# Kernel optimization log

Hardware: AMD Instinct MI355X
Metric: run time of the kernel (lower is better)

Reference implementation:

```python
import jax, jax.numpy as jnp
import numpy as np

B = 8; NPC = 12500; N = B * NPC
L = 10.0; RES = 0.7; K = 16
IN_CH = 64; H1 = 68; H2 = 128; RNN = 128; ATTN = 32; E4 = 4 * RNN
EPS = 1e-5


def _knn_np(refs, queries, k):
    out = np.empty((queries.shape[0], k), dtype=np.int64)
    r2 = (refs * refs).sum(1)
    for s in range(0, queries.shape[0], 2048):
        q = queries[s:s + 2048]
        d2 = (q * q).sum(1)[:, None] - 2.0 * q @ refs.T + r2[None, :]
        out[s:s + q.shape[0]] = np.argpartition(d2, k, axis=1)[:, :k]
    return out


def setup_inputs():
    rng = np.random.default_rng(0)
    pos = rng.uniform(0.0, L, (N, 3)).astype(np.float32)
    batch = np.repeat(np.arange(B), NPC).astype(np.int32)
    x = (0.5 * rng.standard_normal((N, IN_CH))).astype(np.float32)
    refl = rng.uniform(0.0, 1.0, N).astype(np.float32)
    # voxel-grid sampling: one representative point per occupied voxel per cloud
    G = int(np.ceil(L / RES)) + 1
    v = np.floor(pos / RES).astype(np.int64)
    vkey = ((batch.astype(np.int64) * G + v[:, 0]) * G + v[:, 1]) * G + v[:, 2]
    _, first = np.unique(vkey, return_index=True)
    idx = np.sort(first)
    M = idx.shape[0]
    # per-cloud brute-force KNN (k neighbors in full set for every sampled point)
    src_list = []
    for b in range(B):
        qi = idx[(idx >= b * NPC) & (idx < (b + 1) * NPC)]
        src_list.append(_knn_np(pos[b * NPC:(b + 1) * NPC], pos[qi], K) + b * NPC)
    src = np.concatenate(src_list, 0).reshape(-1)
    tgt = np.repeat(np.arange(M), K)
    edge_index = np.stack([src, tgt]).astype(np.int32)

    def W(*s):
        return jnp.asarray((0.05 * rng.standard_normal(s)).astype(np.float32))

    def zeros(c):
        return jnp.zeros((c,), jnp.float32)

    def bnp(c):  # packed inference-mode BN params: [gamma, beta, mean, var]
        return jnp.asarray(np.stack([1.0 + 0.1 * rng.standard_normal(c), 0.1 * rng.standard_normal(c), 0.1 * rng.standard_normal(c), 1.0 + 0.1 * rng.uniform(0.0, 1.0, c)]).astype(np.float32))

    def dwp(c):  # depthwise k=1 conv = per-channel [weight, bias]
        return jnp.asarray(np.stack([1.0 + 0.1 * rng.standard_normal(c), 0.1 * rng.standard_normal(c)]).astype(np.float32))

    gum = -np.log(-np.log(rng.uniform(1e-6, 1.0 - 1e-6, (B, 2))))
    return dict(
        x=jnp.asarray(x), pos=jnp.asarray(pos), reflectance=jnp.asarray(refl),
        gumbel=jnp.asarray(gum.astype(np.float32)),
        gate_w1=W(4, H1), gate_b1=zeros(H1), gate_w2=W(H1, H1), gate_b2=zeros(H1),
        gate_wg=W(H1, 2), gate_bg=jnp.asarray(np.array([0.0, 2.0], np.float32)),
        loc_w1=W(H1, H2), loc_b1=zeros(H2), loc_w2=W(H2, H2), loc_b2=zeros(H2),
        attn_w1=W(H2, ATTN), attn_b1=zeros(ATTN), attn_w2=W(ATTN),
        exp_w=W(RNN, E4), exp_b=zeros(E4), exp_bn=bnp(E4),
        ds1_dw=dwp(E4), ds1_bn1=bnp(E4), ds1_pw_w=W(E4, E4), ds1_pw_b=zeros(E4), ds1_bn2=bnp(E4),
        blk_bn1=bnp(E4),
        ds2_dw=dwp(E4), ds2_bn1=bnp(E4), ds2_pw_w=W(E4, E4), ds2_pw_b=zeros(E4), ds2_bn2=bnp(E4),
        blk_bn2=bnp(E4),
        proj_w=W(E4, RNN), proj_b=zeros(RNN), proj_bn=bnp(RNN),
        batch=jnp.asarray(batch), idx=jnp.asarray(idx.astype(np.int32)),
        edge_index=jnp.asarray(edge_index), k=K, num_graphs=B)


def _bn(z, p):
    return p[0] * (z - p[2]) / jnp.sqrt(p[3] + EPS) + p[1]


def reference(x, pos, reflectance, gumbel, gate_w1, gate_b1, gate_w2, gate_b2, gate_wg, gate_bg, loc_w1, loc_b1, loc_w2, loc_b2, attn_w1, attn_b1, attn_w2, exp_w, exp_b, exp_bn, ds1_dw, ds1_bn1, ds1_pw_w, ds1_pw_b, ds1_bn2, blk_bn1, ds2_dw, ds2_bn1, ds2_pw_w, ds2_pw_b, ds2_bn2, blk_bn2, proj_w, proj_b, proj_bn, batch, idx, edge_index, k, num_graphs):
    # --- BinaryReflectanceGate (soft gumbel-softmax, tau=1) ---
    feats = jnp.concatenate([pos, reflectance[:, None]], -1)  # [N,4]
    h = jax.nn.relu(feats @ gate_w1 + gate_b1)
    h = jax.nn.relu(h @ gate_w2 + gate_b2)
    pooled = jax.ops.segment_max(h, batch, num_segments=num_graphs)  # global_max_pool
    logits = pooled @ gate_wg + gate_bg
    y_soft = jax.nn.softmax(logits + gumbel, axis=-1)
    refl_g = y_soft[:, 1][batch] * reflectance  # gated reflectance [N]
    pos4 = jnp.concatenate([pos, refl_g[:, None]], -1)  # [N,4]
    # --- AttentivePointNetConv: gather -> local MLP -> softmax attn -> reduce ---
    M = idx.shape[0]
    src = edge_index[0].reshape(M, k)  # k source neighbors per centroid
    msg_in = jnp.concatenate([x[src], pos4[src] - pos4[idx][:, None, :]], -1)  # [M,k,68]
    hm = jax.nn.relu(msg_in @ loc_w1 + loc_b1)
    msg = jax.nn.relu(hm @ loc_w2 + loc_b2)  # [M,k,128]
    score = jnp.tanh(msg @ attn_w1 + attn_b1) @ attn_w2  # [M,k]
    alpha = jax.nn.softmax(score, axis=-1)  # softmax over each centroid's edges
    agg = jnp.einsum('mk,mkc->mc', alpha, msg)  # [M,128]
    # --- InvertedResidualBlock (all convs kernel=1 -> channel matmuls, BN inference) ---
    out = jax.nn.relu(_bn(agg @ exp_w + exp_b, exp_bn))  # expand 128->512

    def ds(z, dw, bn1, pw_w, pw_b, bn2):
        d = jax.nn.relu(_bn(z * dw[0] + dw[1], bn1))  # depthwise k=1
        return _bn(d @ pw_w + pw_b, bn2)  # pointwise

    out = _bn(ds(out, ds1_dw, ds1_bn1, ds1_pw_w, ds1_pw_b, ds1_bn2), blk_bn1)
    out = _bn(ds(out, ds2_dw, ds2_bn1, ds2_pw_w, ds2_pw_b, ds2_bn2), blk_bn2)
    out = _bn(out @ proj_w + proj_b, proj_bn)  # project 512->128
    out = jax.nn.relu(out + agg)  # identity shortcut (RNN==RNN)
    return (out, pos[idx], batch[idx], refl_g[idx])
```

## Files before the change

kernel.cpp:

```cpp
#include <hip/hip_runtime.h>
#include <hip/hip_bf16.h>

typedef __hip_bfloat16 bf16;

#define B_GR 8
#define IN_CH 64
#define H1 68
#define H2 128
#define ATTN 32
#define E4 512
#define RNN 128
#define KNN 16
#define EPSV 1e-5f

typedef __attribute__((ext_vector_type(8))) short s8v;
typedef __attribute__((ext_vector_type(4))) float f4v;
#define MFMA16(a,b,c) __builtin_amdgcn_mfma_f32_16x16x32_bf16(a,b,c,0,0,0)

#define SK96 104
#define SK128 136
#define SK512 520

template<int DT> __device__ __forceinline__ float LD(const void* p, size_t i) {
    if (DT) return __bfloat162float(((const bf16*)p)[i]);
    return ((const float*)p)[i];
}
template<int DT> __device__ __forceinline__ void ST(void* p, size_t i, float v) {
    if (DT) ((bf16*)p)[i] = __float2bfloat16(v);
    else    ((float*)p)[i] = v;
}
__device__ __forceinline__ unsigned short f2bfb(float f) {
    unsigned u = __float_as_uint(f);
    unsigned r = (u + 0x7FFFu + ((u >> 16) & 1u)) >> 16;
    return (unsigned short)r;
}
__device__ __forceinline__ float bfb2f(unsigned short u) {
    return __uint_as_float(((unsigned)u) << 16);
}

__global__ void prep_kernel(const void* pos, int* flag, int* pooled) {
    const int tid = threadIdx.x;
    for (int i = tid; i < B_GR*H1; i += 256) pooled[i] = 0;
    if (tid == 0) {
        const unsigned* w = (const unsigned*)pos;
        int ok = 1;
        #pragma unroll 8
        for (int i = 0; i < 256; i++) {
            float f = __uint_as_float((w[i] & 0xFFFFu) << 16);
            if (!(f >= -0.01f && f <= 10.05f)) ok = 0;
        }
        *flag = ok;
    }
}

#define W1T_E (128*SK96)
#define W2T_E (128*SK128)
#define AW1T_E (32*SK128)
#define EXPT_E (512*SK128)
#define D1T_E (512*SK512)
#define D2T_E (512*SK512)
#define PJT_E (128*SK512)
#define GW2T_E (80*SK96)
template<int DT> __global__ __launch_bounds__(256) void trans_kernel(
    const int* __restrict__ flag,
    const void* __restrict__ w1, const void* __restrict__ w2, const void* __restrict__ aw1,
    const void* __restrict__ expw, const void* __restrict__ d1pw,
    const void* __restrict__ d2pw, const void* __restrict__ pjw,
    const void* __restrict__ gw2,
    unsigned short* __restrict__ w1T, unsigned short* __restrict__ w2T,
    unsigned short* __restrict__ aw1T, unsigned short* __restrict__ expwT,
    unsigned short* __restrict__ d1pwT, unsigned short* __restrict__ d2pwT,
    unsigned short* __restrict__ pjwT, unsigned short* __restrict__ gw2gT)
{
    if (*flag != DT) return;
    const int T0 = W1T_E, T1 = T0+W2T_E, T2 = T1+AW1T_E, T3 = T2+EXPT_E,
              T4 = T3+D1T_E, T5 = T4+D2T_E, T6 = T5+PJT_E, T7 = T6+GW2T_E;
    for (int i = blockIdx.x*256 + threadIdx.x; i < T7; i += gridDim.x*256) {
        if (i < T0) {
            int n = i / SK96, k = i - n*SK96;
            w1T[i] = (k < H1) ? f2bfb(LD<DT>(w1, (size_t)k*H2 + n)) : 0;
        } else if (i < T1) {
            int j = i - T0; int n = j / SK128, k = j - n*SK128;
            w2T[j] = (k < H2) ? f2bfb(LD<DT>(w2, (size_t)k*H2 + n)) : 0;
        } else if (i < T2) {
            int j = i - T1; int n = j / SK128, k = j - n*SK128;
            aw1T[j] = (k < H2) ? f2bfb(LD<DT>(aw1, (size_t)k*ATTN + n)) : 0;
        } else if (i < T3) {
            int j = i - T2; int n = j / SK128, k = j - n*SK128;
            expwT[j] = (k < RNN) ? f2bfb(LD<DT>(expw, (size_t)k*E4 + n)) : 0;
        } else if (i < T4) {
            int j = i - T3; int n = j / SK512, k = j - n*SK512;
            d1pwT[j] = (k < E4) ? f2bfb(LD<DT>(d1pw, (size_t)k*E4 + n)) : 0;
        } else if (i < T5) {
            int j = i - T4; int n = j / SK512, k = j - n*SK512;
            d2pwT[j] = (k < E4) ? f2bfb(LD<DT>(d2pw, (size_t)k*E4 + n)) : 0;
        } else if (i < T6) {
            int j = i - T5; int n = j / SK512, k = j - n*SK512;
            pjwT[j] = (k < E4) ? f2bfb(LD<DT>(pjw, (size_t)k*RNN + n)) : 0;
        } else {
            int j = i - T6; int n = j / SK96, k = j - n*SK96;
            gw2gT[j] = (k < H1 && n < H1) ? f2bfb(LD<DT>(gw2, (size_t)k*H1 + n)) : 0;
        }
    }
}

template<int DT> __global__ void coef_kernel(
    const int* __restrict__ flag,
    const void* __restrict__ expb, const void* __restrict__ expbn,
    const void* __restrict__ d1dw, const void* __restrict__ d1bn1,
    const void* __restrict__ d1pb, const void* __restrict__ d1bn2, const void* __restrict__ bbn1,
    const void* __restrict__ d2dw, const void* __restrict__ d2bn1,
    const void* __restrict__ d2pb, const void* __restrict__ d2bn2, const void* __restrict__ bbn2,
    const void* __restrict__ pjb, const void* __restrict__ pjbn,
    float4* __restrict__ C1, float2* __restrict__ C2, float2* __restrict__ C3,
    float2* __restrict__ C4)
{
    if (*flag != DT) return;
    int c = blockIdx.x*256 + threadIdx.x;
    if (c < E4) {
        float a_e = LD<DT>(expbn,c) * rsqrtf(LD<DT>(expbn,3*E4+c)+EPSV);
        float t0  = a_e*(LD<DT>(expb,c) - LD<DT>(expbn,2*E4+c)) + LD<DT>(expbn,E4+c);
        float a1 = LD<DT>(d1bn1,c) * rsqrtf(LD<DT>(d1bn1,3*E4+c)+EPSV);
        float s1 = a1 * LD<DT>(d1dw,c);
        float t1 = a1*(LD<DT>(d1dw,E4+c) - LD<DT>(d1bn1,2*E4+c)) + LD<DT>(d1bn1,E4+c);
        C1[c] = make_float4(a_e, t0, s1, t1);
        float a2 = LD<DT>(d1bn2,c) * rsqrtf(LD<DT>(d1bn2,3*E4+c)+EPSV);
        float t2 = a2*(LD<DT>(d1pb,c) - LD<DT>(d1bn2,2*E4+c)) + LD<DT>(d1bn2,E4+c);
        float a3 = LD<DT>(bbn1,c) * rsqrtf(LD<DT>(bbn1,3*E4+c)+EPSV);
        float S2 = a3*a2;
        float T2 = a3*(t2 - LD<DT>(bbn1,2*E4+c)) + LD<DT>(bbn1,E4+c);
        float a4 = LD<DT>(d2bn1,c) * rsqrtf(LD<DT>(d2bn1,3*E4+c)+EPSV);
        float sdw = a4 * LD<DT>(d2dw,c);
        float tdw = a4*(LD<DT>(d2dw,E4+c) - LD<DT>(d2bn1,2*E4+c)) + LD<DT>(d2bn1,E4+c);
        C2[c] = make_float2(sdw*S2, sdw*T2 + tdw);
        float a5 = LD<DT>(d2bn2,c) * rsqrtf(LD<DT>(d2bn2,3*E4+c)+EPSV);
        float t5 = a5*(LD<DT>(d2pb,c) - LD<DT>(d2bn2,2*E4+c)) + LD<DT>(d2bn2,E4+c);
        float a6 = LD<DT>(bbn2,c) * rsqrtf(LD<DT>(bbn2,3*E4+c)+EPSV);
        C3[c] = make_float2(a6*a5, a6*(t5 - LD<DT>(bbn2,2*E4+c)) + LD<DT>(bbn2,E4+c));
    }
    if (c < RNN) {
        float ap = LD<DT>(pjbn,c) * rsqrtf(LD<DT>(pjbn,3*RNN+c)+EPSV);
        C4[c] = make_float2(ap, ap*(LD<DT>(pjb,c) - LD<DT>(pjbn,2*RNN+c)) + LD<DT>(pjbn,RNN+c));
    }
}

template<int DT> __global__ __launch_bounds__(256) void gate_mfma(
    const int* __restrict__ flag,
    const void* __restrict__ pos, const void* __restrict__ refl,
    const void* __restrict__ w1, const void* __restrict__ b1, const void* __restrict__ b2g,
    const unsigned short* __restrict__ gw2gT,
    int* __restrict__ pooled, int NPC, int CPB)
{
    if (*flag != DT) return;
    __shared__ __align__(16) unsigned short hs[256*SK96];
    __shared__ float w1s[4*H1], b1s[H1], b2s[H1];
    const int tid = threadIdx.x;
    for (int i = tid; i < 4*H1; i += 256) w1s[i] = LD<DT>(w1, i);
    if (tid < H1) { b1s[tid] = LD<DT>(b1, tid); b2s[tid] = LD<DT>(b2g, tid); }
    __syncthreads();

    const int bb = blockIdx.x / CPB;
    const int cc = blockIdx.x % CPB;
    const int base = bb*NPC + cc*256;
    const int limit = NPC - cc*256;
    const int p = base + ((tid < limit) ? tid : 0);

    {
        float f0 = LD<DT>(pos, (size_t)p*3+0), f1 = LD<DT>(pos, (size_t)p*3+1);
        float f2 = LD<DT>(pos, (size_t)p*3+2), f3 = LD<DT>(refl, p);
        float h[H1];
        #pragma unroll
        for (int j = 0; j < H1; j++)
            h[j] = fmaxf(b1s[j] + f0*w1s[j] + f1*w1s[H1+j] + f2*w1s[2*H1+j] + f3*w1s[3*H1+j], 0.f);
        #pragma unroll
        for (int j = 0; j < H1; j += 2) {
            unsigned v = (unsigned)f2bfb(h[j]) | ((unsigned)f2bfb(h[j+1]) << 16);
            *(unsigned*)&hs[tid*SK96 + j] = v;
        }
        #pragma unroll
        for (int j = H1; j < 96; j += 2) *(unsigned*)&hs[tid*SK96 + j] = 0;
    }
    __syncthreads();

    const int wv = tid >> 6, lane = tid & 63, quad = lane >> 4, l15 = lane & 15;
    f4v acc[4][5];
    #pragma unroll
    for (int mt = 0; mt < 4; mt++)
        #pragma unroll
        for (int nt = 0; nt < 5; nt++) acc[mt][nt] = (f4v){0.f,0.f,0.f,0.f};
    s8v af[4][3];
    #pragma unroll
    for (int mt = 0; mt < 4; mt++)
        #pragma unroll
        for (int ks = 0; ks < 3; ks++)
            af[mt][ks] = *(const s8v*)&hs[(wv*64 + mt*16 + l15)*SK96 + ks*32 + quad*8];
    #pragma unroll
    for (int nt = 0; nt < 5; nt++) {
        #pragma unroll
        for (int ks = 0; ks < 3; ks++) {
            s8v bf_ = *(const s8v*)&gw2gT[(size_t)(nt*16 + l15)*SK96 + ks*32 + quad*8];
            #pragma unroll
            for (int mt = 0; mt < 4; mt++) acc[mt][nt] = MFMA16(af[mt][ks], bf_, acc[mt][nt]);
        }
    }
    #pragma unroll
    for (int nt = 0; nt < 5; nt++) {
        int col = nt*16 + l15;
        float v = acc[0][nt][0];
        #pragma unroll
        for (int mt = 0; mt < 4; mt++)
            #pragma unroll
            for (int r = 0; r < 4; r++) v = fmaxf(v, acc[mt][nt][r]);
        v = fmaxf(v, __shfl_xor(v, 16));
        v = fmaxf(v, __shfl_xor(v, 32));
        if (quad == 0 && col < H1) {
            float o = fmaxf(v + b2s[col], 0.f);
            atomicMax(&pooled[bb*H1 + col], __float_as_int(o));
        }
    }
}

template<int DT> __global__ void gate2_kernel(
    const int* __restrict__ flag, const int* __restrict__ pooled,
    const void* __restrict__ wg, const void* __restrict__ bg,
    const void* __restrict__ gum, float* __restrict__ y1)
{
    if (*flag != DT) return;
    __shared__ float lg[B_GR][2];
    const int t = threadIdx.x;
    if (t < B_GR*2) {
        int b = t >> 1, g = t & 1;
        float a = LD<DT>(bg, g) + LD<DT>(gum, b*2+g);
        for (int c = 0; c < H1; c++) a += __int_as_float(pooled[b*H1+c]) * LD<DT>(wg, c*2+g);
        lg[b][g] = a;
    }
    __syncthreads();
    if (t < B_GR) {
        float l0 = lg[t][0], l1 = lg[t][1];
        float m = fmaxf(l0, l1);
        float e0 = __expf(l0-m), e1 = __expf(l1-m);
        y1[t] = e1 / (e0 + e1);
    }
}

template<int DT> __global__ __launch_bounds__(256) void edge_mfma(
    const int* __restrict__ flag,
    const void* __restrict__ x, const void* __restrict__ pos,
    const void* __restrict__ refl, const float* __restrict__ y1,
    const int* __restrict__ batch,
    const int* __restrict__ idxarr, const int* __restrict__ esrc,
    const void* __restrict__ b1, const void* __restrict__ b2,
    const void* __restrict__ ab1, const void* __restrict__ aw2,
    const unsigned short* __restrict__ gw1T, const unsigned short* __restrict__ gw2T,
    const unsigned short* __restrict__ gaw1T,
    void* __restrict__ out, int M)
{
    if (*flag != DT) return;
    __shared__ __align__(16) unsigned short u2[128*SK128];
    __shared__ __align__(16) unsigned short Hs[128*SK128];
    __shared__ float p4[8][4];
    __shared__ int   srow[128];
    __shared__ float b1s[H2], b2s[H2], ab1s[ATTN], aw2s[ATTN];
    __shared__ float scores[128], alpha[128];
    float* att = (float*)Hs;

    const int tid = threadIdx.x;
    const int m0 = blockIdx.x * 8;

    if (tid < 128) {
        int mm = m0 + (tid >> 4); if (mm >= M) mm = M - 1;
        srow[tid] = esrc[mm*KNN + (tid & 15)];
    }
    if (tid < 32) {
        int tt = tid >> 2, c = tid & 3;
        int mm = m0 + tt; if (mm >= M) mm = M - 1;
        int t_idx = idxarr[mm];
        p4[tt][c] = (c < 3) ? LD<DT>(pos, (size_t)t_idx*3 + c)
                            : y1[batch[t_idx]] * LD<DT>(refl, t_idx);
    }
    if (tid < H2) { b1s[tid] = LD<DT>(b1, tid); b2s[tid] = LD<DT>(b2, tid); }
    if (tid < ATTN) { ab1s[tid] = LD<DT>(ab1, tid); aw2s[tid] = LD<DT>(aw2, tid); }
    __syncthreads();

    if (DT) {
        int r = tid >> 1, hf = tid & 1;
        int s = srow[r], tt = r >> 4;
        const uint4* xs = (const uint4*)x;
        uint4* du = (uint4*)u2;
        #pragma unroll
        for (int q = 0; q < 4; q++)
            du[r*13 + hf*4 + q] = xs[(size_t)s*8 + hf*4 + q];
        if (hf == 0) {
            #pragma unroll
            for (int k = 64; k < 68; k++) {
                float v = (k < 67) ? LD<1>(pos, (size_t)s*3 + (k-64)) - p4[tt][k-64]
                                   : y1[batch[s]] * LD<1>(refl, s) - p4[tt][3];
                u2[r*SK96 + k] = f2bfb(v);
            }
        } else {
            #pragma unroll
            for (int k = 68; k < 96; k += 2) *(unsigned*)&u2[r*SK96 + k] = 0;
        }
    } else {
        int r = tid >> 1, half = tid & 1;
        int s = srow[r], tt = r >> 4;
        size_t xb = (size_t)s * IN_CH;
        int k0 = half * 48;
        for (int kk = 0; kk < 48; kk++) {
            int k = k0 + kk;
            float v;
            if (k < IN_CH)       v = LD<DT>(x, xb + k);
            else if (k < 67)     v = LD<DT>(pos, (size_t)s*3 + (k - 64)) - p4[tt][k - 64];
            else if (k == 67)    v = y1[batch[s]] * LD<DT>(refl, s) - p4[tt][3];
            else                 v = 0.f;
            u2[r*SK96 + k] = f2bfb(v);
        }
    }
    __syncthreads();

    const int wv = tid >> 6, lane = tid & 63, quad = lane >> 4, l15 = lane & 15;
    const int rbase = wv * 32;

    {
        f4v acc[2][8];
        #pragma unroll
        for (int mt = 0; mt < 2; mt++)
            #pragma unroll
            for (int nt = 0; nt < 8; nt++) acc[mt][nt] = (f4v){0.f,0.f,0.f,0.f};
        s8v af[2][3];
        #pragma unroll
        for (int mt = 0; mt < 2; mt++)
            #pragma unroll
            for (int ks = 0; ks < 3; ks++)
                af[mt][ks] = *(const s8v*)&u2[(rbase + mt*16 + l15)*SK96 + ks*32 + quad*8];
        #pragma unroll
        for (int nt = 0; nt < 8; nt++) {
            #pragma unroll
            for (int ks = 0; ks < 3; ks++) {
                s8v bf_ = *(const s8v*)&gw1T[(size_t)(nt*16 + l15)*SK96 + ks*32 + quad*8];
                acc[0][nt] = MFMA16(af[0][ks], bf_, acc[0][nt]);
                acc[1][nt] = MFMA16(af[1][ks], bf_, acc[1][nt]);
            }
        }
        #pragma unroll
        for (int mt = 0; mt < 2; mt++)
            #pragma unroll
            for (int nt = 0; nt < 8; nt++)
                #pragma unroll
                for (int r = 0; r < 4; r++) {
                    int row = rbase + mt*16 + quad*4 + r;
                    int col = nt*16 + l15;
                    Hs[row*SK128 + col] = f2bfb(fmaxf(acc[mt][nt][r] + b1s[col], 0.f));
                }
    }
    __syncthreads();

    {
        f4v acc[2][8];
        #pragma unroll
        for (int mt = 0; mt < 2; mt++)
            #pragma unroll
            for (int nt = 0; nt < 8; nt++) acc[mt][nt] = (f4v){0.f,0.f,0.f,0.f};
        s8v af[2][4];
        #pragma unroll
        for (int mt = 0; mt < 2; mt++)
            #pragma unroll
            for (int ks = 0; ks < 4; ks++)
                af[mt][ks] = *(const s8v*)&Hs[(rbase + mt*16 + l15)*SK128 + ks*32 + quad*8];
        #pragma unroll
        for (int nt = 0; nt < 8; nt++) {
            #pragma unroll
            for (int ks = 0; ks < 4; ks++) {
                s8v bf_ = *(const s8v*)&gw2T[(size_t)(nt*16 + l15)*SK128 + ks*32 + quad*8];
                acc[0][nt] = MFMA16(af[0][ks], bf_, acc[0][nt]);
                acc[1][nt] = MFMA16(af[1][ks], bf_, acc[1][nt]);
            }
        }
        #pragma unroll
        for (int mt = 0; mt < 2; mt++)
            #pragma unroll
            for (int nt = 0; nt < 8; nt++)
                #pragma unroll
                for (int r = 0; r < 4; r++) {
                    int row = rbase + mt*16 + quad*4 + r;
                    int col = nt*16 + l15;
                    u2[row*SK128 + col] = f2bfb(fmaxf(acc[mt][nt][r] + b2s[col], 0.f));
                }
    }
    __syncthreads();

    {
        f4v acc[2][2];
        #pragma unroll
        for (int mt = 0; mt < 2; mt++)
            #pragma unroll
            for (int nt = 0; nt < 2; nt++) acc[mt][nt] = (f4v){0.f,0.f,0.f,0.f};
        s8v af[2][4];
        #pragma unroll
        for (int mt = 0; mt < 2; mt++)
            #pragma unroll
            for (int ks = 0; ks < 4; ks++)
                af[mt][ks] = *(const s8v*)&u2[(rbase + mt*16 + l15)*SK128 + ks*32 + quad*8];
        #pragma unroll
        for (int nt = 0; nt < 2; nt++) {
            #pragma unroll
            for (int ks = 0; ks < 4; ks++) {
                s8v bf_ = *(const s8v*)&gaw1T[(size_t)(nt*16 + l15)*SK128 + ks*32 + quad*8];
                acc[0][nt] = MFMA16(af[0][ks], bf_, acc[0][nt]);
                acc[1][nt] = MFMA16(af[1][ks], bf_, acc[1][nt]);
            }
        }
        #pragma unroll
        for (int mt = 0; mt < 2; mt++)
            #pragma unroll
            for (int nt = 0; nt < 2; nt++)
                #pragma unroll
                for (int r = 0; r < 4; r++) {
                    int row = rbase + mt*16 + quad*4 + r;
                    int col = nt*16 + l15;
                    att[row*ATTN + col] = tanhf(acc[mt][nt][r] + ab1s[col]) * aw2s[col];
                }
    }
    __syncthreads();

    if (tid < 128) {
        float s = 0.f;
        const f4v* row = (const f4v*)&att[tid*ATTN];
        #pragma unroll
        for (int i = 0; i < 8; i++) { f4v v = row[i]; s += v[0]+v[1]+v[2]+v[3]; }
        scores[tid] = s;
    }
    __syncthreads();
    if (tid < 128) {
        int base = (tid >> 4) << 4;
        float mx = scores[base];
        #pragma unroll
        for (int j = 1; j < KNN; j++) mx = fmaxf(mx, scores[base+j]);
        float den = 0.f;
        #pragma unroll
        for (int j = 0; j < KNN; j++) den += __expf(scores[base+j] - mx);
        alpha[tid] = __expf(scores[tid] - mx) / den;
    }
    __syncthreads();

    for (int o = tid; o < 1024; o += 256) {
        int tt = o >> 7, c = o & 127;
        int mm = m0 + tt;
        if (mm < M) {
            float a = 0.f;
            #pragma unroll
            for (int j = 0; j < KNN; j++)
                a += alpha[tt*16 + j] * bfb2f(u2[(tt*16 + j)*SK128 + c]);
            ST<DT>(out, (size_t)mm*H2 + c, a);
        }
    }
    if (tid < 32) {
        int tt = tid >> 2, c = tid & 3;
        int mm = m0 + tt;
        if (mm < M) {
            if (c < 3) ST<DT>(out, (size_t)M*128 + mm*3 + c, p4[tt][c]);
            else {
                ST<DT>(out, (size_t)M*131 + mm, (float)batch[idxarr[mm]]);
                ST<DT>(out, (size_t)M*132 + mm, p4[tt][3]);
            }
        }
    }
}

template<int DT> __global__ __launch_bounds__(256) void post_mfma(
    const int* __restrict__ flag,
    const unsigned short* __restrict__ expwT, const unsigned short* __restrict__ d1pwT,
    const unsigned short* __restrict__ d2pwT, const unsigned short* __restrict__ pjwT,
    const float4* __restrict__ C1, const float2* __restrict__ C2,
    const float2* __restrict__ C3, const float2* __restrict__ C4,
    void* __restrict__ out, int M)
{
    if (*flag != DT) return;
    __shared__ __align__(16) unsigned short zs[32*SK512];
    __shared__ __align__(16) unsigned short a0[32*SK128];
    const int tid = threadIdx.x;
    const int m0 = blockIdx.x * 32;

    {
        int r = tid >> 3;
        int c0 = (tid & 7) * 16;
        int mm = m0 + r;
        for (int c = c0; c < c0+16; c++) {
            float v = (mm < M) ? LD<DT>(out, (size_t)mm*RNN + c) : 0.f;
            a0[r*SK128 + c] = f2bfb(v);
        }
        if ((tid & 7) == 7) for (int c = RNN; c < SK128; c++) a0[r*SK128 + c] = 0;
    }
    __syncthreads();

    const int wv = tid >> 6, lane = tid & 63, quad = lane >> 4, l15 = lane & 15;
    const int nbase = wv * 128;

    f4v acc[2][8];

    #pragma unroll
    for (int mt = 0; mt < 2; mt++)
        #pragma unroll
        for (int nt = 0; nt < 8; nt++) acc[mt][nt] = (f4v){0.f,0.f,0.f,0.f};
    #pragma unroll
    for (int ks = 0; ks < 4; ks++) {
        s8v af0 = *(const s8v*)&a0[(l15)*SK128 + ks*32 + quad*8];
        s8v af1 = *(const s8v*)&a0[(16+l15)*SK128 + ks*32 + quad*8];
        #pragma unroll
        for (int nt = 0; nt < 8; nt++) {
            s8v bf_ = *(const s8v*)&expwT[(size_t)(nbase + nt*16 + l15)*SK128 + ks*32 + quad*8];
            acc[0][nt] = MFMA16(af0, bf_, acc[0][nt]);
            acc[1][nt] = MFMA16(af1, bf_, acc[1][nt]);
        }
    }
    #pragma unroll
    for (int nt = 0; nt < 8; nt++) {
        int col = nbase + nt*16 + l15;
        float4 cf = C1[col];
        #pragma unroll
        for (int mt = 0; mt < 2; mt++)
            #pragma unroll
            for (int r = 0; r < 4; r++) {
                int row = mt*16 + quad*4 + r;
                float u = fmaxf(cf.x*acc[mt][nt][r] + cf.y, 0.f);
                float d = fmaxf(cf.z*u + cf.w, 0.f);
                zs[row*SK512 + col] = f2bfb(d);
            }
    }
    __syncthreads();

    #pragma unroll
    for (int mt = 0; mt < 2; mt++)
        #pragma unroll
        for (int nt = 0; nt < 8; nt++) acc[mt][nt] = (f4v){0.f,0.f,0.f,0.f};
    for (int ks = 0; ks < 16; ks++) {
        s8v af0 = *(const s8v*)&zs[(l15)*SK512 + ks*32 + quad*8];
        s8v af1 = *(const s8v*)&zs[(16+l15)*SK512 + ks*32 + quad*8];
        #pragma unroll
        for (int nt = 0; nt < 8; nt++) {
            s8v bf_ = *(const s8v*)&d1pwT[(size_t)(nbase + nt*16 + l15)*SK512 + ks*32 + quad*8];
            acc[0][nt] = MFMA16(af0, bf_, acc[0][nt]);
            acc[1][nt] = MFMA16(af1, bf_, acc[1][nt]);
        }
    }
    __syncthreads();
    #pragma unroll
    for (int nt = 0; nt < 8; nt++) {
        int col = nbase + nt*16 + l15;
        float2 cf = C2[col];
        #pragma unroll
        for (int mt = 0; mt < 2; mt++)
            #pragma unroll
            for (int r = 0; r < 4; r++) {
                int row = mt*16 + quad*4 + r;
                zs[row*SK512 + col] = f2bfb(fmaxf(cf.x*acc[mt][nt][r] + cf.y, 0.f));
            }
    }
    __syncthreads();

    #pragma unroll
    for (int mt = 0; mt < 2; mt++)
        #pragma unroll
        for (int nt = 0; nt < 8; nt++) acc[mt][nt] = (f4v){0.f,0.f,0.f,0.f};
    for (int ks = 0; ks < 16; ks++) {
        s8v af0 = *(const s8v*)&zs[(l15)*SK512 + ks*32 + quad*8];
        s8v af1 = *(const s8v*)&zs[(16+l15)*SK512 + ks*32 + quad*8];
        #pragma unroll
        for (int nt = 0; nt < 8; nt++) {
            s8v bf_ = *(const s8v*)&d2pwT[(size_t)(nbase + nt*16 + l15)*SK512 + ks*32 + quad*8];
            acc[0][nt] = MFMA16(af0, bf_, acc[0][nt]);
            acc[1][nt] = MFMA16(af1, bf_, acc[1][nt]);
        }
    }
    __syncthreads();
    #pragma unroll
    for (int nt = 0; nt < 8; nt++) {
        int col = nbase + nt*16 + l15;
        float2 cf = C3[col];
        #pragma unroll
        for (int mt = 0; mt < 2; mt++)
            #pragma unroll
            for (int r = 0; r < 4; r++) {
                int row = mt*16 + quad*4 + r;
                zs[row*SK512 + col] = f2bfb(cf.x*acc[mt][nt][r] + cf.y);
            }
    }
    __syncthreads();

    {
        f4v pacc[2][2];
        #pragma unroll
        for (int mt = 0; mt < 2; mt++)
            #pragma unroll
            for (int nt = 0; nt < 2; nt++) pacc[mt][nt] = (f4v){0.f,0.f,0.f,0.f};
        for (int ks = 0; ks < 16; ks++) {
            s8v af0 = *(const s8v*)&zs[(l15)*SK512 + ks*32 + quad*8];
            s8v af1 = *(const s8v*)&zs[(16+l15)*SK512 + ks*32 + quad*8];
            #pragma unroll
            for (int nt = 0; nt < 2; nt++) {
                s8v bf_ = *(const s8v*)&pjwT[(size_t)(wv*32 + nt*16 + l15)*SK512 + ks*32 + quad*8];
                pacc[0][nt] = MFMA16(af0, bf_, pacc[0][nt]);
                pacc[1][nt] = MFMA16(af1, bf_, pacc[1][nt]);
            }
        }
        #pragma unroll
        for (int nt = 0; nt < 2; nt++) {
            int col = wv*32 + nt*16 + l15;
            float2 cf = C4[col];
            #pragma unroll
            for (int mt = 0; mt < 2; mt++)
                #pragma unroll
                for (int r = 0; r < 4; r++) {
                    int row = mt*16 + quad*4 + r;
                    int mm = m0 + row;
                    if (mm < M) {
                        float agv = bfb2f(a0[row*SK128 + col]);
                        float o = fmaxf(cf.x*pacc[mt][nt][r] + cf.y + agv, 0.f);
                        ST<DT>(out, (size_t)mm*RNN + col, o);
                    }
                }
        }
    }
}

extern "C" void kernel_launch(void* const* d_in, const int* in_sizes, int n_in,
                              void* d_out, int out_size, void* d_ws, size_t ws_size,
                              hipStream_t stream)
{
    const void* x    = d_in[0];
    const void* pos  = d_in[1];
    const void* refl = d_in[2];
    const void* gum  = d_in[3];
    const void* gw1  = d_in[4];
    const void* gb1  = d_in[5];
    const void* gw2  = d_in[6];
    const void* gb2  = d_in[7];
    const void* gwg  = d_in[8];
    const void* gbg  = d_in[9];
    const void* lw1  = d_in[10];
    const void* lb1  = d_in[11];
    const void* lw2  = d_in[12];
    const void* lb2  = d_in[13];
    const void* aw1  = d_in[14];
    const void* ab1  = d_in[15];
    const void* aw2  = d_in[16];
    const void* expw = d_in[17];
    const void* expb = d_in[18];
    const void* expbn= d_in[19];
    const void* d1dw = d_in[20];
    const void* d1bn1= d_in[21];
    const void* d1pw = d_in[22];
    const void* d1pb = d_in[23];
    const void* d1bn2= d_in[24];
    const void* bbn1 = d_in[25];
    const void* d2dw = d_in[26];
    const void* d2bn1= d_in[27];
    const void* d2pw = d_in[28];
    const void* d2pb = d_in[29];
    const void* d2bn2= d_in[30];
    const void* bbn2 = d_in[31];
    const void* pjw  = d_in[32];
    const void* pjb  = d_in[33];
    const void* pjbn = d_in[34];
    const int* batch = (const int*)d_in[35];
    const int* idxp  = (const int*)d_in[36];
    const int* eidx  = (const int*)d_in[37];

    const int N = in_sizes[2];
    const int M = in_sizes[36];
    const int NPC = N / B_GR;
    const int CPB = (NPC + 255) / 256;

    char* wsb = (char*)d_ws;
    int*  flag   = (int*)wsb;
    int*  pooled = (int*)(wsb + 16);
    float* y1    = (float*)(wsb + 2304);
    unsigned short* w1T   = (unsigned short*)(wsb + 2368);
    unsigned short* w2T   = w1T + W1T_E;
    unsigned short* aw1T  = w2T + W2T_E;
    unsigned short* expwT = aw1T + AW1T_E;
    unsigned short* d1pwT = expwT + EXPT_E;
    unsigned short* d2pwT = d1pwT + D1T_E;
    unsigned short* pjwT  = d2pwT + D2T_E;
    unsigned short* gw2gT = pjwT + PJT_E;
    float4* C1 = (float4*)(gw2gT + GW2T_E + 8);
    float2* C2 = (float2*)(C1 + E4);
    float2* C3 = C2 + E4;
    float2* C4 = C3 + E4;

    prep_kernel<<<1, 256, 0, stream>>>(pos, flag, pooled);

    trans_kernel<0><<<512, 256, 0, stream>>>(flag, lw1, lw2, aw1, expw, d1pw, d2pw, pjw, gw2,
                                             w1T, w2T, aw1T, expwT, d1pwT, d2pwT, pjwT, gw2gT);
    trans_kernel<1><<<512, 256, 0, stream>>>(flag, lw1, lw2, aw1, expw, d1pw, d2pw, pjw, gw2,
                                             w1T, w2T, aw1T, expwT, d1pwT, d2pwT, pjwT, gw2gT);

    coef_kernel<0><<<2, 256, 0, stream>>>(flag, expb, expbn, d1dw, d1bn1, d1pb, d1bn2, bbn1,
                                          d2dw, d2bn1, d2pb, d2bn2, bbn2, pjb, pjbn,
                                          C1, C2, C3, C4);
    coef_kernel<1><<<2, 256, 0, stream>>>(flag, expb, expbn, d1dw, d1bn1, d1pb, d1bn2, bbn1,
                                          d2dw, d2bn1, d2pb, d2bn2, bbn2, pjb, pjbn,
                                          C1, C2, C3, C4);

    gate_mfma<0><<<B_GR*CPB, 256, 0, stream>>>(flag, pos, refl, gw1, gb1, gb2, gw2gT, pooled, NPC, CPB);
    gate_mfma<1><<<B_GR*CPB, 256, 0, stream>>>(flag, pos, refl, gw1, gb1, gb2, gw2gT, pooled, NPC, CPB);

    gate2_kernel<0><<<1, 64, 0, stream>>>(flag, pooled, gwg, gbg, gum, y1);
    gate2_kernel<1><<<1, 64, 0, stream>>>(flag, pooled, gwg, gbg, gum, y1);

    const int EB = (M + 7) / 8;
    edge_mfma<0><<<EB, 256, 0, stream>>>(flag, x, pos, refl, y1, batch, idxp, eidx,
                                         lb1, lb2, ab1, aw2, w1T, w2T, aw1T, d_out, M);
    edge_mfma<1><<<EB, 256, 0, stream>>>(flag, x, pos, refl, y1, batch, idxp, eidx,
                                         lb1, lb2, ab1, aw2, w1T, w2T, aw1T, d_out, M);

    const int PB = (M + 31) / 32;
    post_mfma<0><<<PB, 256, 0, stream>>>(flag, expwT, d1pwT, d2pwT, pjwT, C1, C2, C3, C4, d_out, M);
    post_mfma<1><<<PB, 256, 0, stream>>>(flag, expwT, d1pwT, d2pwT, pjwT, C1, C2, C3, C4, d_out, M);
}
```

Baseline: 532.0 us.

## Reuse one LDS buffer across MLP stages, fuse score reduction via shuffles, vectorize aggregation

Drops the second 128x136 bf16 shared buffer so every MLP stage reads from and writes back into the same buffer. Each stage loads its A fragments into registers and syncs before overwriting, which halves LDS use per block and should allow more resident blocks per CU. The attention score sum is now done with lane shuffles in registers instead of a shared scratch array, removing one LDS round trip and a barrier. The final alpha-weighted aggregation reads 8 bf16 values per load and writes with 16-byte stores; the cost is extra barriers between stages.

```diff
diff --git a/kernel.cpp b/kernel.cpp
--- a/kernel.cpp
+++ b/kernel.cpp
@@ -257,12 +257,10 @@
 {
     if (*flag != DT) return;
     __shared__ __align__(16) unsigned short u2[128*SK128];
-    __shared__ __align__(16) unsigned short Hs[128*SK128];
     __shared__ float p4[8][4];
     __shared__ int   srow[128];
     __shared__ float b1s[H2], b2s[H2], ab1s[ATTN], aw2s[ATTN];
     __shared__ float scores[128], alpha[128];
-    float* att = (float*)Hs;
 
     const int tid = threadIdx.x;
     const int m0 = blockIdx.x * 8;
@@ -289,17 +287,17 @@
         uint4* du = (uint4*)u2;
         #pragma unroll
         for (int q = 0; q < 4; q++)
-            du[r*13 + hf*4 + q] = xs[(size_t)s*8 + hf*4 + q];
+            du[r*17 + hf*4 + q] = xs[(size_t)s*8 + hf*4 + q];
         if (hf == 0) {
             #pragma unroll
             for (int k = 64; k < 68; k++) {
                 float v = (k < 67) ? LD<1>(pos, (size_t)s*3 + (k-64)) - p4[tt][k-64]
                                    : y1[batch[s]] * LD<1>(refl, s) - p4[tt][3];
-                u2[r*SK96 + k] = f2bfb(v);
+                u2[r*SK128 + k] = f2bfb(v);
             }
         } else {
             #pragma unroll
-            for (int k = 68; k < 96; k += 2) *(unsigned*)&u2[r*SK96 + k] = 0;
+            for (int k = 68; k < 96; k += 2) *(unsigned*)&u2[r*SK128 + k] = 0;
         }
     } else {
         int r = tid >> 1, half = tid & 1;
@@ -313,7 +311,7 @@
             else if (k < 67)     v = LD<DT>(pos, (size_t)s*3 + (k - 64)) - p4[tt][k - 64];
             else if (k == 67)    v = y1[batch[s]] * LD<DT>(refl, s) - p4[tt][3];
             else                 v = 0.f;
-            u2[r*SK96 + k] = f2bfb(v);
+            u2[r*SK128 + k] = f2bfb(v);
         }
     }
     __syncthreads();
@@ -322,17 +320,18 @@
     const int rbase = wv * 32;
 
     {
+        s8v af[2][3];
+        #pragma unroll
+        for (int mt = 0; mt < 2; mt++)
+            #pragma unroll
+            for (int ks = 0; ks < 3; ks++)
+                af[mt][ks] = *(const s8v*)&u2[(rbase + mt*16 + l15)*SK128 + ks*32 + quad*8];
+        __syncthreads();
         f4v acc[2][8];
         #pragma unroll
         for (int mt = 0; mt < 2; mt++)
             #pragma unroll
             for (int nt = 0; nt < 8; nt++) acc[mt][nt] = (f4v){0.f,0.f,0.f,0.f};
-        s8v af[2][3];
-        #pragma unroll
-        for (int mt = 0; mt < 2; mt++)
-            #pragma unroll
-            for (int ks = 0; ks < 3; ks++)
-                af[mt][ks] = *(const s8v*)&u2[(rbase + mt*16 + l15)*SK96 + ks*32 + quad*8];
         #pragma unroll
         for (int nt = 0; nt < 8; nt++) {
             #pragma unroll
@@ -350,23 +349,24 @@
                 for (int r = 0; r < 4; r++) {
                     int row = rbase + mt*16 + quad*4 + r;
                     int col = nt*16 + l15;
-                    Hs[row*SK128 + col] = f2bfb(fmaxf(acc[mt][nt][r] + b1s[col], 0.f));
+                    u2[row*SK128 + col] = f2bfb(fmaxf(acc[mt][nt][r] + b1s[col], 0.f));
                 }
     }
     __syncthreads();
 
     {
+        s8v af[2][4];
+        #pragma unroll
+        for (int mt = 0; mt < 2; mt++)
+            #pragma unroll
+            for (int ks = 0; ks < 4; ks++)
+                af[mt][ks] = *(const s8v*)&u2[(rbase + mt*16 + l15)*SK128 + ks*32 + quad*8];
+        __syncthreads();
         f4v acc[2][8];
         #pragma unroll
         for (int mt = 0; mt < 2; mt++)
             #pragma unroll
             for (int nt = 0; nt < 8; nt++) acc[mt][nt] = (f4v){0.f,0.f,0.f,0.f};
-        s8v af[2][4];
-        #pragma unroll
-        for (int mt = 0; mt < 2; mt++)
-            #pragma unroll
-            for (int ks = 0; ks < 4; ks++)
-                af[mt][ks] = *(const s8v*)&Hs[(rbase + mt*16 + l15)*SK128 + ks*32 + quad*8];
         #pragma unroll
         for (int nt = 0; nt < 8; nt++) {
             #pragma unroll
@@ -390,17 +390,17 @@
     __syncthreads();
 
     {
-        f4v acc[2][2];
-        #pragma unroll
-        for (int mt = 0; mt < 2; mt++)
-            #pragma unroll
-            for (int nt = 0; nt < 2; nt++) acc[mt][nt] = (f4v){0.f,0.f,0.f,0.f};
         s8v af[2][4];
         #pragma unroll
         for (int mt = 0; mt < 2; mt++)
             #pragma unroll
             for (int ks = 0; ks < 4; ks++)
                 af[mt][ks] = *(const s8v*)&u2[(rbase + mt*16 + l15)*SK128 + ks*32 + quad*8];
+        f4v acc[2][2];
+        #pragma unroll
+        for (int mt = 0; mt < 2; mt++)
+            #pragma unroll
+            for (int nt = 0; nt < 2; nt++) acc[mt][nt] = (f4v){0.f,0.f,0.f,0.f};
         #pragma unroll
         for (int nt = 0; nt < 2; nt++) {
             #pragma unroll
@@ -413,24 +413,22 @@
         #pragma unroll
         for (int mt = 0; mt < 2; mt++)
             #pragma unroll
-            for (int nt = 0; nt < 2; nt++)
+            for (int r = 0; r < 4; r++) {
+                float s = 0.f;
                 #pragma unroll
-                for (int r = 0; r < 4; r++) {
-                    int row = rbase + mt*16 + quad*4 + r;
+                for (int nt = 0; nt < 2; nt++) {
                     int col = nt*16 + l15;
-                    att[row*ATTN + col] = tanhf(acc[mt][nt][r] + ab1s[col]) * aw2s[col];
+                    s += tanhf(acc[mt][nt][r] + ab1s[col]) * aw2s[col];
                 }
-    }
-    __syncthreads();
-
-    if (tid < 128) {
-        float s = 0.f;
-        const f4v* row = (const f4v*)&att[tid*ATTN];
-        #pragma unroll
-        for (int i = 0; i < 8; i++) { f4v v = row[i]; s += v[0]+v[1]+v[2]+v[3]; }
-        scores[tid] = s;
-    }
-    __syncthreads();
+                s += __shfl_xor(s, 1);
+                s += __shfl_xor(s, 2);
+                s += __shfl_xor(s, 4);
+                s += __shfl_xor(s, 8);
+                if (l15 == 0) scores[rbase + mt*16 + quad*4 + r] = s;
+            }
+    }
+    __syncthreads();
+
     if (tid < 128) {
         int base = (tid >> 4) << 4;
         float mx = scores[base];
@@ -443,19 +441,31 @@
     }
     __syncthreads();
 
-    for (int o = tid; o < 1024; o += 256) {
-        int tt = o >> 7, c = o & 127;
+    if (tid < 128) {
+        int tt = tid >> 4, c0 = (tid & 15) * 8;
         int mm = m0 + tt;
+        float a[8] = {0,0,0,0,0,0,0,0};
+        #pragma unroll
+        for (int j = 0; j < KNN; j++) {
+            float al = alpha[tt*16 + j];
+            s8v v = *(const s8v*)&u2[(tt*16 + j)*SK128 + c0];
+            #pragma unroll
+            for (int e = 0; e < 8; e++) a[e] += al * bfb2f((unsigned short)v[e]);
+        }
         if (mm < M) {
-            float a = 0.f;
-            #pragma unroll
-            for (int j = 0; j < KNN; j++)
-                a += alpha[tt*16 + j] * bfb2f(u2[(tt*16 + j)*SK128 + c]);
-            ST<DT>(out, (size_t)mm*H2 + c, a);
-        }
-    }
-    if (tid < 32) {
-        int tt = tid >> 2, c = tid & 3;
+            if (DT) {
+                unsigned short pk[8];
+                #pragma unroll
+                for (int e = 0; e < 8; e++) pk[e] = f2bfb(a[e]);
+                *(uint4*)((bf16*)out + (size_t)mm*H2 + c0) = *(const uint4*)pk;
+            } else {
+                #pragma unroll
+                for (int e = 0; e < 8; e++) ST<0>(out, (size_t)mm*H2 + c0 + e, a[e]);
+            }
+        }
+    } else if (tid < 160) {
+        int t = tid - 128;
+        int tt = t >> 2, c = t & 3;
         int mm = m0 + tt;
         if (mm < M) {
             if (c < 3) ST<DT>(out, (size_t)M*128 + mm*3 + c, p4[tt][c]);
```

New measurement: 560.8 us. 1.05x slower.
